# Optimization experiments

Measured on AMD Instinct MI355X. Metric: run time of the kernel, lower is better.

The kernel has to match this reference:

```python
import jax, jax.numpy as jnp
import numpy as np

B, S, D = 4, 2048, 1024
H, DK, DV = 16, 64, 64


def setup_inputs() -> dict:
    key = jax.random.key(0)
    ks = jax.random.split(key, 12)
    scale = 1.0 / np.sqrt(D)
    queries = jax.random.normal(ks[0], (B, S, D), dtype=jnp.float32)
    keys_ = jax.random.normal(ks[1], (B, S, D), dtype=jnp.float32)
    values = jax.random.normal(ks[2], (B, S, D), dtype=jnp.float32)
    # binary additive mask (1 = masked out), broadcastable over batch and heads
    mask = jax.random.randint(ks[3], (1, 1, S, S), 0, 2).astype(jnp.float32)
    Wq = jax.random.normal(ks[4], (D, H * DK), dtype=jnp.float32) * scale
    bq = jnp.zeros((H * DK,), dtype=jnp.float32)
    Wk = jax.random.normal(ks[5], (D, H * DK), dtype=jnp.float32) * scale
    bk = jnp.zeros((H * DK,), dtype=jnp.float32)
    Wv = jax.random.normal(ks[6], (D, H * DV), dtype=jnp.float32) * scale
    bv = jnp.zeros((H * DV,), dtype=jnp.float32)
    Wo = jax.random.normal(ks[7], (H * DV, D), dtype=jnp.float32) * scale
    bo = jnp.zeros((D,), dtype=jnp.float32)
    return {"queries": queries, "keys": keys_, "values": values, "mask": mask,
            "Wq": Wq, "bq": bq, "Wk": Wk, "bk": bk, "Wv": Wv, "bv": bv,
            "Wo": Wo, "bo": bo}


def reference(queries, keys, values, mask, Wq, bq, Wk, bk, Wv, bv, Wo, bo):
    b = queries.shape[0]
    # projections + split heads: [B, S, H*Dh] -> [B, H, S, Dh]
    q = (queries @ Wq + bq).reshape(b, -1, H, DK).transpose(0, 2, 1, 3)
    k = (keys @ Wk + bk).reshape(b, -1, H, DK).transpose(0, 2, 1, 3)
    v = (values @ Wv + bv).reshape(b, -1, H, DV).transpose(0, 2, 1, 3)
    scores = jnp.einsum("bhqd,bhkd->bhqk", q, k) / jnp.sqrt(jnp.float32(DK))
    scores = scores + mask * (-1e9)
    attn = jax.nn.softmax(scores, axis=-1)
    ctx = jnp.einsum("bhqk,bhkd->bhqd", attn, v)  # [B, H, S, DV]
    ctx = ctx.transpose(0, 2, 1, 3).reshape(b, -1, H * DV)
    return ctx @ Wo + bo
```

## Files before the change

kernel.cpp:

```cpp
#include <hip/hip_runtime.h>
#include <cstdint>
#include <cstddef>

typedef __attribute__((ext_vector_type(8))) short bf16x8;
typedef __attribute__((ext_vector_type(4))) short bf16x4;
typedef __attribute__((ext_vector_type(4))) float f32x4;

__device__ __forceinline__ unsigned short f2bf(float f) {
    union { float f; unsigned int u; } v; v.f = f;
    unsigned int r = v.u + 0x7FFFu + ((v.u >> 16) & 1u);
    return (unsigned short)(r >> 16);
}
__device__ __forceinline__ unsigned int pk2(float a, float b) {
    return (unsigned int)f2bf(a) | ((unsigned int)f2bf(b) << 16);
}
__device__ __forceinline__ unsigned int pkfast(float a, float b) {
    unsigned int ua = __builtin_bit_cast(unsigned int, a) + 0x8000u;
    unsigned int ub = __builtin_bit_cast(unsigned int, b) + 0x8000u;
    return __builtin_amdgcn_perm(ub, ua, 0x07060302u);
}

typedef __attribute__((address_space(1))) void gvoid;
typedef __attribute__((address_space(3))) void svoid;
__device__ __forceinline__ void ld16_lds(const void* g, void* l) {
    __builtin_amdgcn_global_load_lds((gvoid*)g, (svoid*)l, 16, 0, 0);
}

#define QSCALE 0.1803368801111204f

__global__ __launch_bounds__(256)
void cvt_bf16(const float* __restrict__ A, const float* __restrict__ B,
              const float* __restrict__ C,
              unsigned short* __restrict__ oa, unsigned short* __restrict__ ob,
              unsigned short* __restrict__ oc)
{
    const float* src = (blockIdx.y == 0) ? A : (blockIdx.y == 1) ? B : C;
    unsigned short* dst = (blockIdx.y == 0) ? oa : (blockIdx.y == 1) ? ob : oc;
    const size_t i = ((size_t)blockIdx.x * 256 + threadIdx.x) * 8;
    float4 a = *(const float4*)(src + i);
    float4 b = *(const float4*)(src + i + 4);
    uint4 p;
    p.x = pk2(a.x, a.y); p.y = pk2(a.z, a.w);
    p.z = pk2(b.x, b.y); p.w = pk2(b.z, b.w);
    *(uint4*)(dst + i) = p;
}

__global__ __launch_bounds__(256)
void prep_weights(const float* __restrict__ W0, const float* __restrict__ W1,
                  const float* __restrict__ W2, const float* __restrict__ W3,
                  unsigned short* __restrict__ T0, unsigned short* __restrict__ T1,
                  unsigned short* __restrict__ T2, unsigned short* __restrict__ T3)
{
    __shared__ float t[32][33];
    const int z = blockIdx.z;
    const float* W = (z == 0) ? W0 : (z == 1) ? W1 : (z == 2) ? W2 : W3;
    unsigned short* Wt = (z == 0) ? T0 : (z == 1) ? T1 : (z == 2) ? T2 : T3;
    const int n0 = blockIdx.x * 32, k0 = blockIdx.y * 32;
    const int tx = threadIdx.x & 31, ty = threadIdx.x >> 5;
#pragma unroll
    for (int i = 0; i < 4; i++)
        t[ty + 8 * i][tx] = W[(size_t)(k0 + ty + 8 * i) * 1024 + n0 + tx];
    __syncthreads();
#pragma unroll
    for (int i = 0; i < 4; i++)
        Wt[(size_t)(n0 + ty + 8 * i) * 1024 + k0 + tx] = f2bf(t[tx][ty + 8 * i]);
}

__global__ __launch_bounds__(256)
void mask_pack(const float* __restrict__ m, unsigned long long* __restrict__ bits)
{
    const int wv = (blockIdx.x << 2) | (threadIdx.x >> 6);
    const int lane = threadIdx.x & 63;
    for (int i = 0; i < 64; i++) {
        const size_t word = (size_t)wv * 64 + i;
        const float v = m[word * 64 + lane];
        unsigned long long b = __ballot(v != 0.0f);
        if (lane == 0) bits[word] = b;
    }
}

template <int MODE>
__global__ __launch_bounds__(256, 2)
void gemm128(const unsigned short* __restrict__ A,
             const unsigned short* __restrict__ Wt, const float* __restrict__ bias,
             unsigned short* __restrict__ ob, float* __restrict__ of)
{
    __shared__ __align__(16) unsigned short sm[(MODE == 2) ? 18432 : 8192];
    unsigned short* As = sm;
    unsigned short* Bs = sm + 4096;

    const int tid  = threadIdx.x;
    const int lane = tid & 63;
    const int wave = tid >> 6;
    const int quad = lane >> 4;
    const int l16  = lane & 15;
    const int wr   = wave >> 1;
    const int wc   = wave & 1;

    const int m0 = blockIdx.x * 128;
    const int n0 = blockIdx.y * 128;

    const int sr0 = tid >> 2,        sc0 = (tid & 3) << 4;
    const int sr1 = sr0 + 64,        sc1 = sc0;

    const char* Ab = (const char*)A  + (size_t)m0 * 2048;
    const char* Bb = (const char*)Wt + (size_t)n0 * 2048;

    f32x4 acc[4][4];
#pragma unroll
    for (int i = 0; i < 4; i++)
#pragma unroll
        for (int j = 0; j < 4; j++) acc[i][j] = (f32x4){0.f, 0.f, 0.f, 0.f};

    for (int kk = 0; kk < 1024; kk += 32) {
        const int kb2 = kk * 2;
        ld16_lds(Ab + (size_t)sr0 * 2048 + kb2 + sc0, (char*)As + tid * 16);
        ld16_lds(Ab + (size_t)sr1 * 2048 + kb2 + sc1, (char*)As + (256 + tid) * 16);
        ld16_lds(Bb + (size_t)sr0 * 2048 + kb2 + sc0, (char*)Bs + tid * 16);
        ld16_lds(Bb + (size_t)sr1 * 2048 + kb2 + sc1, (char*)Bs + (256 + tid) * 16);
        __syncthreads();

        bf16x8 af[4], bfr[4];
#pragma unroll
        for (int mt = 0; mt < 4; mt++)
            af[mt] = *(const bf16x8*)&As[(wr * 64 + mt * 16 + l16) * 32 + quad * 8];
#pragma unroll
        for (int nt = 0; nt < 4; nt++)
            bfr[nt] = *(const bf16x8*)&Bs[(wc * 64 + nt * 16 + l16) * 32 + quad * 8];
#pragma unroll
        for (int mt = 0; mt < 4; mt++)
#pragma unroll
            for (int nt = 0; nt < 4; nt++)
                acc[mt][nt] = __builtin_amdgcn_mfma_f32_16x16x32_bf16(af[mt], bfr[nt], acc[mt][nt], 0, 0, 0);
        __syncthreads();
    }

    float bv[4];
#pragma unroll
    for (int nt = 0; nt < 4; nt++) bv[nt] = bias[n0 + wc * 64 + nt * 16 + l16];

    if (MODE == 3) {
#pragma unroll
        for (int mt = 0; mt < 4; mt++) {
            const int m = m0 + wr * 64 + mt * 16 + quad * 4;
#pragma unroll
            for (int nt = 0; nt < 4; nt++) {
                const int n = n0 + wc * 64 + nt * 16 + l16;
#pragma unroll
                for (int r = 0; r < 4; r++)
                    of[(size_t)(m + r) * 1024 + n] = acc[mt][nt][r] + bv[nt];
            }
        }
    } else if (MODE == 0 || MODE == 1) {
#pragma unroll
        for (int mt = 0; mt < 4; mt++) {
            const int m = m0 + wr * 64 + mt * 16 + quad * 4;
            const int b = m >> 11;
#pragma unroll
            for (int nt = 0; nt < 4; nt++) {
                const int n = n0 + wc * 64 + nt * 16 + l16;
                const int h = n >> 6, dk = n & 63;
#pragma unroll
                for (int r = 0; r < 4; r++) {
                    const int s = (m + r) & 2047;
                    float o = acc[mt][nt][r] + bv[nt];
                    if (MODE == 0) o *= QSCALE;
                    ob[((size_t)((b << 4) + h) * 2048 + s) * 64 + dk] = f2bf(o);
                }
            }
        }
    } else {
        unsigned short* T = sm + wave * (64 * 72);
#pragma unroll
        for (int mt = 0; mt < 4; mt++)
#pragma unroll
            for (int nt = 0; nt < 4; nt++)
#pragma unroll
                for (int r = 0; r < 4; r++)
                    T[(nt * 16 + l16) * 72 + mt * 16 + quad * 4 + r] = f2bf(acc[mt][nt][r] + bv[nt]);
        __syncthreads();
#pragma unroll
        for (int i = 0; i < 8; i++) {
            const int nl = i * 8 + (lane >> 3);
            const int mc = lane & 7;
            uint4 v = *(const uint4*)&T[nl * 72 + mc * 8];
            const int n  = n0 + wc * 64 + nl;
            const int mg = m0 + wr * 64 + mc * 8;
            const int b = mg >> 11, s = mg & 2047;
            const int h = n >> 6, dv = n & 63;
            *(uint4*)&ob[((size_t)((b << 4) + h) * 64 + dv) * 2048 + s] = v;
        }
    }
}

__global__ __launch_bounds__(256, 4)
void attn_kernel(const unsigned short* __restrict__ q,
                 const unsigned short* __restrict__ k,
                 const unsigned short* __restrict__ vT,
                 const unsigned int* __restrict__ mbits,
                 unsigned short* __restrict__ ctx)
{
    __shared__ __align__(16) unsigned short Ks[2][64 * 64];
    __shared__ __align__(16) unsigned short Vs[2][64 * 64];

    const int tid = threadIdx.x, lane = tid & 63, wave = tid >> 6;
    const int quad = lane >> 4, l16 = lane & 15;
    const int sw = l16 & 7;
    const int bid = blockIdx.x;
    const int qblk = bid & 15, h = (bid >> 4) & 15, b = bid >> 8;

    const unsigned short* qb = q  + (size_t)(b * 16 + h) * 2048 * 64;
    const unsigned short* kb = k  + (size_t)(b * 16 + h) * 2048 * 64;
    const unsigned short* vb = vT + (size_t)(b * 16 + h) * 64 * 2048;

    const int c0 = tid, c1 = 256 + tid;
    const int r0 = c0 >> 3, gcc0 = (c0 & 7) ^ (r0 & 7);
    const int r1 = c1 >> 3, gcc1 = (c1 & 7) ^ (r1 & 7);

    int qrow[2];
    bf16x8 qf[2][2];
    f32x4 O0[4], O1[4];
    float l_i[2] = {0.f, 0.f};
#pragma unroll
    for (int g = 0; g < 2; g++) {
        qrow[g] = qblk * 128 + wave * 32 + g * 16 + l16;
        qf[g][0] = *(const bf16x8*)&qb[qrow[g] * 64 + quad * 8];
        qf[g][1] = *(const bf16x8*)&qb[qrow[g] * 64 + 32 + quad * 8];
    }
#pragma unroll
    for (int i = 0; i < 4; i++) { O0[i] = (f32x4){0.f,0.f,0.f,0.f}; O1[i] = (f32x4){0.f,0.f,0.f,0.f}; }
    const unsigned int* mrow0 = mbits + (size_t)qrow[0] * 64;
    const unsigned int* mrow1 = mbits + (size_t)qrow[1] * 64;

    {
        ld16_lds((const char*)kb + (size_t)r0 * 128 + gcc0 * 16, (char*)Ks[0] + c0 * 16);
        ld16_lds((const char*)kb + (size_t)r1 * 128 + gcc1 * 16, (char*)Ks[0] + c1 * 16);
        ld16_lds((const char*)vb + (size_t)r0 * 4096 + gcc0 * 16, (char*)Vs[0] + c0 * 16);
        ld16_lds((const char*)vb + (size_t)r1 * 4096 + gcc1 * 16, (char*)Vs[0] + c1 * 16);
    }
    uint2 mwc0 = *(const uint2*)&mrow0[0];
    uint2 mwc1 = *(const uint2*)&mrow1[0];

    for (int it = 0; it < 32; ++it) {
        const int kt = it << 6;
        const int cur = it & 1, nxt = cur ^ 1;
        __syncthreads();

        if (it < 31) {
            const char* kg = (const char*)kb + (size_t)(kt + 64) * 128;
            const char* vg = (const char*)vb + (size_t)(kt + 64) * 2;
            ld16_lds(kg + (size_t)r0 * 128 + gcc0 * 16, (char*)Ks[nxt] + c0 * 16);
            ld16_lds(kg + (size_t)r1 * 128 + gcc1 * 16, (char*)Ks[nxt] + c1 * 16);
            ld16_lds(vg + (size_t)r0 * 4096 + gcc0 * 16, (char*)Vs[nxt] + c0 * 16);
            ld16_lds(vg + (size_t)r1 * 4096 + gcc1 * 16, (char*)Vs[nxt] + c1 * 16);
        }
        const int mi = (it < 31) ? ((kt + 64) >> 5) : 0;
        uint2 mwn0 = *(const uint2*)&mrow0[mi];
        uint2 mwn1 = *(const uint2*)&mrow1[mi];

        const unsigned short* Kc = Ks[cur];
        const unsigned short* Vc = Vs[cur];

        f32x4 S0[4], S1[4];
#pragma unroll
        for (int mt = 0; mt < 4; mt++) {
            const unsigned short* kp = Kc + (mt * 16 + l16) * 64;
            bf16x8 ka0 = *(const bf16x8*)&kp[((quad    ) ^ sw) * 8];
            bf16x8 ka1 = *(const bf16x8*)&kp[((4 + quad) ^ sw) * 8];
            f32x4 z0 = (f32x4){0.f,0.f,0.f,0.f};
            f32x4 z1 = (f32x4){0.f,0.f,0.f,0.f};
            z0 = __builtin_amdgcn_mfma_f32_16x16x32_bf16(ka0, qf[0][0], z0, 0, 0, 0);
            S0[mt] = __builtin_amdgcn_mfma_f32_16x16x32_bf16(ka1, qf[0][1], z0, 0, 0, 0);
            z1 = __builtin_amdgcn_mfma_f32_16x16x32_bf16(ka0, qf[1][0], z1, 0, 0, 0);
            S1[mt] = __builtin_amdgcn_mfma_f32_16x16x32_bf16(ka1, qf[1][1], z1, 0, 0, 0);
        }
        float sum0 = 0.f, sum1 = 0.f;
        bf16x4 pf0[4], pf1[4];
#pragma unroll
        for (int mt = 0; mt < 4; mt++) {
            const unsigned int wm0 = ((mt & 2) ? mwc0.y : mwc0.x) >> (((mt & 1) << 4) + (quad << 2));
            const unsigned int wm1 = ((mt & 2) ? mwc1.y : mwc1.x) >> (((mt & 1) << 4) + (quad << 2));
#pragma unroll
            for (int r = 0; r < 4; r++) {
                float s0 = ((wm0 >> r) & 1u) ? -1e8f : S0[mt][r];
                float s1 = ((wm1 >> r) & 1u) ? -1e8f : S1[mt][r];
                s0 = __builtin_amdgcn_exp2f(s0);
                s1 = __builtin_amdgcn_exp2f(s1);
                S0[mt][r] = s0; sum0 += s0;
                S1[mt][r] = s1; sum1 += s1;
            }
            uint2 u0, u1;
            u0.x = pkfast(S0[mt][0], S0[mt][1]); u0.y = pkfast(S0[mt][2], S0[mt][3]);
            u1.x = pkfast(S1[mt][0], S1[mt][1]); u1.y = pkfast(S1[mt][2], S1[mt][3]);
            pf0[mt] = __builtin_bit_cast(bf16x4, u0);
            pf1[mt] = __builtin_bit_cast(bf16x4, u1);
        }
        l_i[0] += sum0; l_i[1] += sum1;

#pragma unroll
        for (int dvt = 0; dvt < 4; dvt++) {
            const unsigned short* vp = Vc + (dvt * 16 + l16) * 64;
#pragma unroll
            for (int mt = 0; mt < 4; mt++) {
                uint2 vv = *(const uint2*)&vp[((2 * mt + (quad >> 1)) ^ sw) * 8 + (quad & 1) * 4];
                bf16x4 va = __builtin_bit_cast(bf16x4, vv);
                O0[dvt] = __builtin_amdgcn_mfma_f32_16x16x16bf16_1k(va, pf0[mt], O0[dvt], 0, 0, 0);
                O1[dvt] = __builtin_amdgcn_mfma_f32_16x16x16bf16_1k(va, pf1[mt], O1[dvt], 0, 0, 0);
            }
        }
        mwc0 = mwn0; mwc1 = mwn1;
    }
#pragma unroll
    for (int g = 0; g < 2; g++) {
        float lsum = l_i[g];
        lsum += __shfl_xor(lsum, 16);
        lsum += __shfl_xor(lsum, 32);
        const float rl = __builtin_amdgcn_rcpf(lsum);
        const f32x4* O = g ? O1 : O0;
#pragma unroll
        for (int dvt = 0; dvt < 4; dvt++) {
            uint2 st;
            st.x = pk2(O[dvt][0] * rl, O[dvt][1] * rl);
            st.y = pk2(O[dvt][2] * rl, O[dvt][3] * rl);
            *(uint2*)&ctx[(size_t)(b * 2048 + qrow[g]) * 1024 + h * 64 + dvt * 16 + quad * 4] = st;
        }
    }
}

extern "C" void kernel_launch(void* const* d_in, const int* in_sizes, int n_in,
                              void* d_out, int out_size, void* d_ws, size_t ws_size,
                              hipStream_t stream)
{
    const float* Qin = (const float*)d_in[0];
    const float* Kin = (const float*)d_in[1];
    const float* Vin = (const float*)d_in[2];
    const float* Msk = (const float*)d_in[3];
    const float* Wq  = (const float*)d_in[4];
    const float* bq  = (const float*)d_in[5];
    const float* Wk  = (const float*)d_in[6];
    const float* bk  = (const float*)d_in[7];
    const float* Wv  = (const float*)d_in[8];
    const float* bv  = (const float*)d_in[9];
    const float* Wo  = (const float*)d_in[10];
    const float* bo  = (const float*)d_in[11];

    unsigned short* w = (unsigned short*)d_ws;
    unsigned short* wtq  = w;
    unsigned short* wtk  = w + (1u << 20);
    unsigned short* wtv  = w + 2u * (1u << 20);
    unsigned short* wto  = w + 3u * (1u << 20);
    unsigned short* qcv  = w + 4u * (1u << 20);
    unsigned short* kcv  = qcv + (1u << 23);
    unsigned short* vcv  = kcv + (1u << 23);
    unsigned short* qb   = vcv + (1u << 23);
    unsigned short* kb   = qb  + (1u << 23);
    unsigned short* vTb  = kb  + (1u << 23);
    unsigned short* ctxb = qcv;
    unsigned long long* mb = (unsigned long long*)(vTb + (1u << 23));

    prep_weights<<<dim3(32, 32, 4), 256, 0, stream>>>(Wq, Wk, Wv, Wo, wtq, wtk, wtv, wto);
    mask_pack<<<256, 256, 0, stream>>>(Msk, mb);
    cvt_bf16<<<dim3(4096, 3), 256, 0, stream>>>(Qin, Kin, Vin, qcv, kcv, vcv);
    gemm128<0><<<dim3(64, 8), 256, 0, stream>>>(qcv, wtq, bq, qb, nullptr);
    gemm128<1><<<dim3(64, 8), 256, 0, stream>>>(kcv, wtk, bk, kb, nullptr);
    gemm128<2><<<dim3(64, 8), 256, 0, stream>>>(vcv, wtv, bv, vTb, nullptr);
    attn_kernel<<<1024, 256, 0, stream>>>(qb, kb, vTb, (const unsigned int*)mb, ctxb);
    gemm128<3><<<dim3(64, 8), 256, 0, stream>>>(ctxb, wto, bo, nullptr, (float*)d_out);
}
```

Measured before the change: 422.6 us.

## Double-buffer GEMM tiles, merge QKV projections into one launch, vectorize mask packing

The GEMM main loop now double-buffers the LDS tiles, so the next K-slice is prefetched while MFMAs run on the current one, with one barrier per iteration instead of two. The three Q/K/V projection GEMMs become a single launch with blockIdx.z picking the operands. This relies on the contiguous workspace layout of the inputs, weights and outputs. Mask packing now has each thread read 8 floats with vector loads and write a byte, instead of ballot loops. The cost is twice the LDS per block, which can lower occupancy.

```diff
diff --git a/kernel.cpp b/kernel.cpp
--- a/kernel.cpp
+++ b/kernel.cpp
@@ -67,44 +67,46 @@
 }
 
 __global__ __launch_bounds__(256)
-void mask_pack(const float* __restrict__ m, unsigned long long* __restrict__ bits)
-{
-    const int wv = (blockIdx.x << 2) | (threadIdx.x >> 6);
-    const int lane = threadIdx.x & 63;
-    for (int i = 0; i < 64; i++) {
-        const size_t word = (size_t)wv * 64 + i;
-        const float v = m[word * 64 + lane];
-        unsigned long long b = __ballot(v != 0.0f);
-        if (lane == 0) bits[word] = b;
-    }
-}
-
-template <int MODE>
-__global__ __launch_bounds__(256, 2)
-void gemm128(const unsigned short* __restrict__ A,
-             const unsigned short* __restrict__ Wt, const float* __restrict__ bias,
-             unsigned short* __restrict__ ob, float* __restrict__ of)
-{
-    __shared__ __align__(16) unsigned short sm[(MODE == 2) ? 18432 : 8192];
-    unsigned short* As = sm;
-    unsigned short* Bs = sm + 4096;
-
-    const int tid  = threadIdx.x;
-    const int lane = tid & 63;
-    const int wave = tid >> 6;
-    const int quad = lane >> 4;
-    const int l16  = lane & 15;
-    const int wr   = wave >> 1;
-    const int wc   = wave & 1;
-
-    const int m0 = blockIdx.x * 128;
-    const int n0 = blockIdx.y * 128;
-
-    const int sr0 = tid >> 2,        sc0 = (tid & 3) << 4;
-    const int sr1 = sr0 + 64,        sc1 = sc0;
+void mask_pack(const float* __restrict__ m, unsigned char* __restrict__ bits)
+{
+    const size_t i = ((size_t)blockIdx.x * 256 + threadIdx.x) * 8;
+    float4 a = *(const float4*)(m + i);
+    float4 b = *(const float4*)(m + i + 4);
+    unsigned c = 0;
+    c |= (a.x != 0.f) ? 1u : 0u;
+    c |= (a.y != 0.f) ? 2u : 0u;
+    c |= (a.z != 0.f) ? 4u : 0u;
+    c |= (a.w != 0.f) ? 8u : 0u;
+    c |= (b.x != 0.f) ? 16u : 0u;
+    c |= (b.y != 0.f) ? 32u : 0u;
+    c |= (b.z != 0.f) ? 64u : 0u;
+    c |= (b.w != 0.f) ? 128u : 0u;
+    bits[i >> 3] = (unsigned char)c;
+}
+
+__global__ __launch_bounds__(256, 3)
+void qkv_gemm(const unsigned short* __restrict__ A0,
+              const unsigned short* __restrict__ W0,
+              const float* __restrict__ bq, const float* __restrict__ bk,
+              const float* __restrict__ bv,
+              unsigned short* __restrict__ out0)
+{
+    __shared__ __align__(16) unsigned short sm[18432];
+
+    const int z = blockIdx.z;
+    const unsigned short* A  = A0 + ((size_t)z << 23);
+    const unsigned short* Wt = W0 + ((size_t)z << 20);
+    const float* bias = (z == 0) ? bq : (z == 1) ? bk : bv;
+    unsigned short* ob = out0 + ((size_t)z << 23);
+
+    const int tid = threadIdx.x, lane = tid & 63, wave = tid >> 6;
+    const int quad = lane >> 4, l16 = lane & 15;
+    const int wr = wave >> 1, wc = wave & 1;
+    const int m0 = blockIdx.x * 128, n0 = blockIdx.y * 128;
 
     const char* Ab = (const char*)A  + (size_t)m0 * 2048;
     const char* Bb = (const char*)Wt + (size_t)n0 * 2048;
+    const int sr0 = tid >> 2, sc0 = (tid & 3) << 4;
 
     f32x4 acc[4][4];
 #pragma unroll
@@ -112,13 +114,29 @@
 #pragma unroll
         for (int j = 0; j < 4; j++) acc[i][j] = (f32x4){0.f, 0.f, 0.f, 0.f};
 
-    for (int kk = 0; kk < 1024; kk += 32) {
-        const int kb2 = kk * 2;
-        ld16_lds(Ab + (size_t)sr0 * 2048 + kb2 + sc0, (char*)As + tid * 16);
-        ld16_lds(Ab + (size_t)sr1 * 2048 + kb2 + sc1, (char*)As + (256 + tid) * 16);
-        ld16_lds(Bb + (size_t)sr0 * 2048 + kb2 + sc0, (char*)Bs + tid * 16);
-        ld16_lds(Bb + (size_t)sr1 * 2048 + kb2 + sc1, (char*)Bs + (256 + tid) * 16);
+    {
+        char* Ad = (char*)sm;
+        char* Bd = Ad + 8192;
+        ld16_lds(Ab + (size_t)sr0 * 2048 + sc0,        Ad + tid * 16);
+        ld16_lds(Ab + (size_t)(sr0 + 64) * 2048 + sc0, Ad + (256 + tid) * 16);
+        ld16_lds(Bb + (size_t)sr0 * 2048 + sc0,        Bd + tid * 16);
+        ld16_lds(Bb + (size_t)(sr0 + 64) * 2048 + sc0, Bd + (256 + tid) * 16);
+    }
+
+    for (int it = 0; it < 32; ++it) {
+        const int cur = it & 1;
         __syncthreads();
+        if (it < 31) {
+            const int kb2 = (it + 1) * 64;
+            char* Ad = (char*)(sm + (cur ^ 1) * 8192);
+            char* Bd = Ad + 8192;
+            ld16_lds(Ab + (size_t)sr0 * 2048 + kb2 + sc0,        Ad + tid * 16);
+            ld16_lds(Ab + (size_t)(sr0 + 64) * 2048 + kb2 + sc0, Ad + (256 + tid) * 16);
+            ld16_lds(Bb + (size_t)sr0 * 2048 + kb2 + sc0,        Bd + tid * 16);
+            ld16_lds(Bb + (size_t)(sr0 + 64) * 2048 + kb2 + sc0, Bd + (256 + tid) * 16);
+        }
+        const unsigned short* As = sm + cur * 8192;
+        const unsigned short* Bs = As + 4096;
 
         bf16x8 af[4], bfr[4];
 #pragma unroll
@@ -132,26 +150,13 @@
 #pragma unroll
             for (int nt = 0; nt < 4; nt++)
                 acc[mt][nt] = __builtin_amdgcn_mfma_f32_16x16x32_bf16(af[mt], bfr[nt], acc[mt][nt], 0, 0, 0);
-        __syncthreads();
-    }
-
-    float bv[4];
-#pragma unroll
-    for (int nt = 0; nt < 4; nt++) bv[nt] = bias[n0 + wc * 64 + nt * 16 + l16];
-
-    if (MODE == 3) {
-#pragma unroll
-        for (int mt = 0; mt < 4; mt++) {
-            const int m = m0 + wr * 64 + mt * 16 + quad * 4;
-#pragma unroll
-            for (int nt = 0; nt < 4; nt++) {
-                const int n = n0 + wc * 64 + nt * 16 + l16;
-#pragma unroll
-                for (int r = 0; r < 4; r++)
-                    of[(size_t)(m + r) * 1024 + n] = acc[mt][nt][r] + bv[nt];
-            }
-        }
-    } else if (MODE == 0 || MODE == 1) {
+    }
+
+    float bvv[4];
+#pragma unroll
+    for (int nt = 0; nt < 4; nt++) bvv[nt] = bias[n0 + wc * 64 + nt * 16 + l16];
+
+    if (z < 2) {
 #pragma unroll
         for (int mt = 0; mt < 4; mt++) {
             const int m = m0 + wr * 64 + mt * 16 + quad * 4;
@@ -163,13 +168,14 @@
 #pragma unroll
                 for (int r = 0; r < 4; r++) {
                     const int s = (m + r) & 2047;
-                    float o = acc[mt][nt][r] + bv[nt];
-                    if (MODE == 0) o *= QSCALE;
+                    float o = acc[mt][nt][r] + bvv[nt];
+                    if (z == 0) o *= QSCALE;
                     ob[((size_t)((b << 4) + h) * 2048 + s) * 64 + dk] = f2bf(o);
                 }
             }
         }
     } else {
+        __syncthreads();
         unsigned short* T = sm + wave * (64 * 72);
 #pragma unroll
         for (int mt = 0; mt < 4; mt++)
@@ -177,7 +183,7 @@
             for (int nt = 0; nt < 4; nt++)
 #pragma unroll
                 for (int r = 0; r < 4; r++)
-                    T[(nt * 16 + l16) * 72 + mt * 16 + quad * 4 + r] = f2bf(acc[mt][nt][r] + bv[nt]);
+                    T[(nt * 16 + l16) * 72 + mt * 16 + quad * 4 + r] = f2bf(acc[mt][nt][r] + bvv[nt]);
         __syncthreads();
 #pragma unroll
         for (int i = 0; i < 8; i++) {
@@ -189,6 +195,82 @@
             const int b = mg >> 11, s = mg & 2047;
             const int h = n >> 6, dv = n & 63;
             *(uint4*)&ob[((size_t)((b << 4) + h) * 64 + dv) * 2048 + s] = v;
+        }
+    }
+}
+
+__global__ __launch_bounds__(256, 3)
+void gemm_final(const unsigned short* __restrict__ A,
+                const unsigned short* __restrict__ Wt, const float* __restrict__ bias,
+                float* __restrict__ of)
+{
+    __shared__ __align__(16) unsigned short sm[16384];
+
+    const int tid = threadIdx.x, lane = tid & 63, wave = tid >> 6;
+    const int quad = lane >> 4, l16 = lane & 15;
+    const int wr = wave >> 1, wc = wave & 1;
+    const int m0 = blockIdx.x * 128, n0 = blockIdx.y * 128;
+
+    const char* Ab = (const char*)A  + (size_t)m0 * 2048;
+    const char* Bb = (const char*)Wt + (size_t)n0 * 2048;
+    const int sr0 = tid >> 2, sc0 = (tid & 3) << 4;
+
+    f32x4 acc[4][4];
+#pragma unroll
+    for (int i = 0; i < 4; i++)
+#pragma unroll
+        for (int j = 0; j < 4; j++) acc[i][j] = (f32x4){0.f, 0.f, 0.f, 0.f};
+
+    {
+        char* Ad = (char*)sm;
+        char* Bd = Ad + 8192;
+        ld16_lds(Ab + (size_t)sr0 * 2048 + sc0,        Ad + tid * 16);
+        ld16_lds(Ab + (size_t)(sr0 + 64) * 2048 + sc0, Ad + (256 + tid) * 16);
+        ld16_lds(Bb + (size_t)sr0 * 2048 + sc0,        Bd + tid * 16);
+        ld16_lds(Bb + (size_t)(sr0 + 64) * 2048 + sc0, Bd + (256 + tid) * 16);
+    }
+
+    for (int it = 0; it < 32; ++it) {
+        const int cur = it & 1;
+        __syncthreads();
+        if (it < 31) {
+            const int kb2 = (it + 1) * 64;
+            char* Ad = (char*)(sm + (cur ^ 1) * 8192);
+            char* Bd = Ad + 8192;
+            ld16_lds(Ab + (size_t)sr0 * 2048 + kb2 + sc0,        Ad + tid * 16);
+            ld16_lds(Ab + (size_t)(sr0 + 64) * 2048 + kb2 + sc0, Ad + (256 + tid) * 16);
+            ld16_lds(Bb + (size_t)sr0 * 2048 + kb2 + sc0,        Bd + tid * 16);
+            ld16_lds(Bb + (size_t)(sr0 + 64) * 2048 + kb2 + sc0, Bd + (256 + tid) * 16);
+        }
+        const unsigned short* As = sm + cur * 8192;
+        const unsigned short* Bs = As + 4096;
+
+        bf16x8 af[4], bfr[4];
+#pragma unroll
+        for (int mt = 0; mt < 4; mt++)
+            af[mt] = *(const bf16x8*)&As[(wr * 64 + mt * 16 + l16) * 32 + quad * 8];
+#pragma unroll
+        for (int nt = 0; nt < 4; nt++)
+            bfr[nt] = *(const bf16x8*)&Bs[(wc * 64 + nt * 16 + l16) * 32 + quad * 8];
+#pragma unroll
+        for (int mt = 0; mt < 4; mt++)
+#pragma unroll
+            for (int nt = 0; nt < 4; nt++)
+                acc[mt][nt] = __builtin_amdgcn_mfma_f32_16x16x32_bf16(af[mt], bfr[nt], acc[mt][nt], 0, 0, 0);
+    }
+
+    float bvv[4];
+#pragma unroll
+    for (int nt = 0; nt < 4; nt++) bvv[nt] = bias[n0 + wc * 64 + nt * 16 + l16];
+#pragma unroll
+    for (int mt = 0; mt < 4; mt++) {
+        const int m = m0 + wr * 64 + mt * 16 + quad * 4;
+#pragma unroll
+        for (int nt = 0; nt < 4; nt++) {
+            const int n = n0 + wc * 64 + nt * 16 + l16;
+#pragma unroll
+            for (int r = 0; r < 4; r++)
+                of[(size_t)(m + r) * 1024 + n] = acc[mt][nt][r] + bvv[nt];
         }
     }
 }
@@ -359,11 +441,9 @@
     unsigned long long* mb = (unsigned long long*)(vTb + (1u << 23));
 
     prep_weights<<<dim3(32, 32, 4), 256, 0, stream>>>(Wq, Wk, Wv, Wo, wtq, wtk, wtv, wto);
-    mask_pack<<<256, 256, 0, stream>>>(Msk, mb);
+    mask_pack<<<2048, 256, 0, stream>>>(Msk, (unsigned char*)mb);
     cvt_bf16<<<dim3(4096, 3), 256, 0, stream>>>(Qin, Kin, Vin, qcv, kcv, vcv);
-    gemm128<0><<<dim3(64, 8), 256, 0, stream>>>(qcv, wtq, bq, qb, nullptr);
-    gemm128<1><<<dim3(64, 8), 256, 0, stream>>>(kcv, wtk, bk, kb, nullptr);
-    gemm128<2><<<dim3(64, 8), 256, 0, stream>>>(vcv, wtv, bv, vTb, nullptr);
+    qkv_gemm<<<dim3(64, 8, 3), 256, 0, stream>>>(qcv, wtq, bq, bk, bv, qb);
     attn_kernel<<<1024, 256, 0, stream>>>(qb, kb, vTb, (const unsigned int*)mb, ctxb);
-    gemm128<3><<<dim3(64, 8), 256, 0, stream>>>(ctxb, wto, bo, nullptr, (float*)d_out);
-}
+    gemm_final<<<dim3(64, 8), 256, 0, stream>>>(ctxb, wto, bo, (float*)d_out);
+}
```

Measured after the change: 388.0 us. 1.09x faster.
